# Kernel tuning notes

Hardware: AMD Instinct MI355X
Metric: run time of the kernel (lower is better)

Reference implementation:

```python
import jax, jax.numpy as jnp
import numpy as np

C = 128

def setup_inputs() -> dict:
    key = jax.random.key(0)
    ks = jax.random.split(key, 7)
    x = jax.random.normal(ks[0], (4, 64, 64, C), dtype=jnp.float32)
    s = 1.0 / np.sqrt(C)
    Wq = jax.random.normal(ks[1], (C, C), dtype=jnp.float32) * s
    bq = jnp.zeros((C,), dtype=jnp.float32)
    Wk = jax.random.normal(ks[2], (C, C), dtype=jnp.float32) * s
    bk = jnp.zeros((C,), dtype=jnp.float32)
    Wv = jax.random.normal(ks[3], (C, C), dtype=jnp.float32) * s
    bv = jnp.zeros((C,), dtype=jnp.float32)
    return {"x": x, "Wq": Wq, "bq": bq, "Wk": Wk, "bk": bk, "Wv": Wv, "bv": bv}

def reference(x, Wq, bq, Wk, bk, Wv, bv):
    B, H, W, Cc = x.shape
    N = H * W
    xt = x.reshape(B, N, Cc)  # 1x1 conv == per-token linear
    q = xt @ Wq + bq
    k = xt @ Wk + bk
    v = xt @ Wv + bv
    scale = jnp.sqrt(jnp.asarray(Cc, dtype=x.dtype))
    attn = jnp.einsum('bnc,bmc->bnm', q, k) / scale  # [B, N, N]
    attn = jax.nn.softmax(attn, axis=-1)
    out = jnp.einsum('bnm,bmc->bnc', attn, v)
    return x + out.reshape(B, H, W, Cc)
```

## Files before the change

kernel.cpp:

```cpp
#include <hip/hip_runtime.h>

constexpr int C       = 128;
constexpr int N       = 4096;
constexpr int BATCH   = 4;
constexpr int TOTROWS = BATCH * N;
constexpr float SCALE = 0.08838834764831845f;
constexpr float LOG2E = 1.44269504088896340736f;

constexpr int BK = 64;

typedef __attribute__((ext_vector_type(8))) short        bf16x8;
typedef __attribute__((ext_vector_type(4))) float        f32x4;
typedef __attribute__((ext_vector_type(2))) unsigned int u32x2;

__device__ inline unsigned short f2bf(float f) {
    unsigned int u = __float_as_uint(f);
    return (unsigned short)((u + 0x7FFFu + ((u >> 16) & 1u)) >> 16);
}
__device__ inline unsigned int cvtpk(float a, float b) {
    unsigned int r;
    asm("v_cvt_pk_bf16_f32 %0, %1, %2" : "=v"(r) : "v"(a), "v"(b));
    return r;
}
__device__ inline float bf2f(unsigned int u) {
    return __uint_as_float(u << 16);
}
__device__ inline float fexp2(float x) {
#if __has_builtin(__builtin_amdgcn_exp2f)
    return __builtin_amdgcn_exp2f(x);
#else
    float r; asm("v_exp_f32 %0, %1\n\ts_nop 0" : "=v"(r) : "v"(x)); return r;
#endif
}
__device__ inline void dma16(const void* g, void* l) {
    __builtin_amdgcn_global_load_lds(
        (const __attribute__((address_space(1))) void*)g,
        (__attribute__((address_space(3))) void*)l, 16, 0, 0);
}

__global__ __launch_bounds__(256)
void qkv_kernel(const float* __restrict__ x,
                const float* __restrict__ Wq, const float* __restrict__ bq,
                const float* __restrict__ Wk, const float* __restrict__ bk,
                const float* __restrict__ Wv, const float* __restrict__ bv,
                unsigned short* __restrict__ qo,
                unsigned short* __restrict__ ko,
                unsigned short* __restrict__ vt)
{
    constexpr int TS = 136;
    __shared__ __align__(16) unsigned short wl[128 * TS];

    const int tid  = threadIdx.x;
    const int wv   = tid >> 6;
    const int lane = tid & 63;
    const int lo   = lane & 15;
    const int quad = lane >> 4;
    const int mat  = blockIdx.y;
    const long rowbase = (long)blockIdx.x * 64 + wv * 16;

    const float* W    = (mat == 0) ? Wq : (mat == 1) ? Wk : Wv;
    const float* bias = (mat == 0) ? bq : (mat == 1) ? bk : bv;
    const float  s    = (mat == 0) ? SCALE * LOG2E : 1.0f;

    bf16x8 xf[4];
    {
        const float4* xr = reinterpret_cast<const float4*>(&x[(rowbase + lo) * C]);
        #pragma unroll
        for (int ks = 0; ks < 4; ++ks) {
            float4 a  = xr[ks * 8 + quad * 2];
            float4 b2 = xr[ks * 8 + quad * 2 + 1];
            union { bf16x8 v; unsigned int u[4]; } cv;
            cv.u[0] = cvtpk(a.x, a.y);
            cv.u[1] = cvtpk(a.z, a.w);
            cv.u[2] = cvtpk(b2.x, b2.y);
            cv.u[3] = cvtpk(b2.z, b2.w);
            xf[ks] = cv.v;
        }
    }

    #pragma unroll
    for (int g = 0; g < 16; ++g) {
        int idx = g * 256 + tid;
        int i = idx >> 5, c4 = (idx & 31) * 4;
        float4 a = *reinterpret_cast<const float4*>(&W[i * 128 + c4]);
        wl[(c4 + 0) * TS + i] = f2bf(a.x * s);
        wl[(c4 + 1) * TS + i] = f2bf(a.y * s);
        wl[(c4 + 2) * TS + i] = f2bf(a.z * s);
        wl[(c4 + 3) * TS + i] = f2bf(a.w * s);
    }
    __syncthreads();

    if (mat < 2) {
        f32x4 acc[8] = {};
        #pragma unroll
        for (int ks = 0; ks < 4; ++ks)
            #pragma unroll
            for (int mt = 0; mt < 8; ++mt) {
                bf16x8 wf = *reinterpret_cast<const bf16x8*>(
                    &wl[(mt * 16 + lo) * TS + ks * 32 + quad * 8]);
                acc[mt] = __builtin_amdgcn_mfma_f32_16x16x32_bf16(
                    wf, xf[ks], acc[mt], 0, 0, 0);
            }
        unsigned short* out = (mat == 0) ? qo : ko;
        long row = rowbase + lo;
        #pragma unroll
        for (int mt = 0; mt < 8; ++mt) {
            float4 bb = *reinterpret_cast<const float4*>(&bias[mt * 16 + quad * 4]);
            u32x2 w;
            w[0] = cvtpk(acc[mt][0] + bb.x * s, acc[mt][1] + bb.y * s);
            w[1] = cvtpk(acc[mt][2] + bb.z * s, acc[mt][3] + bb.w * s);
            *reinterpret_cast<u32x2*>(&out[row * C + mt * 16 + quad * 4]) = w;
        }
    } else {
        f32x4 acc[8] = {};
        #pragma unroll
        for (int ks = 0; ks < 4; ++ks)
            #pragma unroll
            for (int ct = 0; ct < 8; ++ct) {
                bf16x8 wf = *reinterpret_cast<const bf16x8*>(
                    &wl[(ct * 16 + lo) * TS + ks * 32 + quad * 8]);
                acc[ct] = __builtin_amdgcn_mfma_f32_16x16x32_bf16(
                    xf[ks], wf, acc[ct], 0, 0, 0);
            }
        const int b = (int)(rowbase >> 12);
        const int nbase = (int)(rowbase & (N - 1));
        const int n0   = nbase + quad * 4;
        const int nblk = n0 >> 6;
        #pragma unroll
        for (int ct = 0; ct < 8; ++ct) {
            int chan = ct * 16 + lo;
            float bb = bias[chan];
            u32x2 w;
            w[0] = cvtpk(acc[ct][0] + bb, acc[ct][1] + bb);
            w[1] = cvtpk(acc[ct][2] + bb, acc[ct][3] + bb);
            *reinterpret_cast<u32x2*>(
                &vt[(((size_t)b * 64 + nblk) * 128 + chan) * 64 + (n0 & 63)]) = w;
        }
    }
}

__global__ __launch_bounds__(256, 2)
void attn_kernel(const unsigned short* __restrict__ q,
                 const unsigned short* __restrict__ k,
                 const unsigned short* __restrict__ vt,
                 unsigned short* __restrict__ opart,
                 float* __restrict__ lpart)
{
    __shared__ __align__(16) unsigned short smA[17472];
    __shared__ __align__(16) unsigned short smB[16384];
    __shared__ __align__(16) unsigned short smP[4096];

    const int tid  = threadIdx.x;
    const int wv   = tid >> 6;
    const int lane = tid & 63;
    const int lo   = lane & 15;
    const int quad = lane >> 4;

    const int nspl = (int)(gridDim.x >> 7);
    const int id   = blockIdx.x;
    int b, sl, qt;
    if (nspl == 4) {
        b  = (id >> 1) & 3;
        sl = (id & 1) | (((id >> 3) & 1) << 1);
        qt = id >> 4;
    } else {
        b  = (id >> 1) & 3;
        sl = id & 1;
        qt = id >> 3;
    }
    const int NIT  = (N / nspl) / BK;
    const int koff = sl * (N / nspl);

    const int    rowb  = b * N + qt * 128;
    const size_t qrow0 = (size_t)rowb + wv * 32;
    const unsigned short* kb  = k  + ((size_t)b * N + koff) * C;
    const unsigned short* vtb = vt + ((size_t)b * 64 + (koff >> 6)) * (size_t)(128 * 64);
    const char* kb8 = (const char*)kb;
    const char* vb8 = (const char*)vtb;

    unsigned short* PW = smP + wv * 1024;

    bf16x8 qf[2][4];
    #pragma unroll
    for (int nt = 0; nt < 2; ++nt)
        #pragma unroll
        for (int ks = 0; ks < 4; ++ks)
            qf[nt][ks] = *reinterpret_cast<const bf16x8*>(
                &q[(qrow0 + nt * 16 + lo) * C + ks * 32 + quad * 8]);

    int offK[4], offV[4];
    #pragma unroll
    for (int c = 0; c < 4; ++c) {
        int G  = (wv * 4 + c) * 64 + lane;
        int kr = G >> 4;
        offK[c] = kr * 256 + (((G & 15) ^ (kr & 7)) << 4);
        int vr = G >> 3;
        offV[c] = vr * 128 + (((G & 7) ^ (vr & 7)) << 4);
    }

    auto stage = [&](int kt, unsigned short* dstKV) {
        const char* kt8 = kb8 + kt * 16384;
        const char* vt8 = vb8 + kt * 16384;
        #pragma unroll
        for (int c = 0; c < 4; ++c)
            dma16(kt8 + offK[c], dstKV + (wv * 4 + c) * 512);
        #pragma unroll
        for (int c = 0; c < 4; ++c)
            dma16(vt8 + offV[c], dstKV + 8192 + (wv * 4 + c) * 512);
    };

    float l_i[2] = { 0.f, 0.f };
    f32x4 ot[2][8] = {};

    auto body = [&](const unsigned short* base) {
        const unsigned short* kc = base;
        const unsigned short* vc = base + 8192;

        f32x4 st[4][2] = {};
        #pragma unroll
        for (int ks = 0; ks < 4; ++ks)
            #pragma unroll
            for (int mt = 0; mt < 4; ++mt) {
                const bf16x8 kf = *reinterpret_cast<const bf16x8*>(
                    &kc[(mt * 16 + lo) * 128 + (((ks * 4 + quad) ^ (lo & 7)) << 3)]);
                #pragma unroll
                for (int nt = 0; nt < 2; ++nt)
                    st[mt][nt] = __builtin_amdgcn_mfma_f32_16x16x32_bf16(
                        kf, qf[nt][ks], st[mt][nt], 0, 0, 0);
            }

        #pragma unroll
        for (int h = 0; h < 2; ++h) {
            #pragma unroll
            for (int nt = 0; nt < 2; ++nt) {
                const int prow = nt * 16 + lo;
                float ps = 0.f;
                #pragma unroll
                for (int m = 0; m < 2; ++m) {
                    f32x4 s = st[2 * h + m][nt];
                    float p0 = fexp2(s[0]);
                    float p1 = fexp2(s[1]);
                    float p2 = fexp2(s[2]);
                    float p3 = fexp2(s[3]);
                    ps += (p0 + p1) + (p2 + p3);
                    u32x2 w;
                    w[0] = cvtpk(p0, p1);
                    w[1] = cvtpk(p2, p3);
                    *reinterpret_cast<u32x2*>(
                        &PW[prow * 32 + (((2 * m + (quad >> 1)) ^ (prow & 3)) << 3)
                            + (quad & 1) * 4]) = w;
                }
                l_i[nt] += ps;
            }
            bf16x8 pf[2];
            #pragma unroll
            for (int nt = 0; nt < 2; ++nt) {
                const int prow = nt * 16 + lo;
                pf[nt] = *reinterpret_cast<const bf16x8*>(
                    &PW[prow * 32 + ((quad ^ (prow & 3)) << 3)]);
            }
            #pragma unroll
            for (int ct = 0; ct < 8; ++ct) {
                const bf16x8 vf = *reinterpret_cast<const bf16x8*>(
                    &vc[(ct * 16 + lo) * 64 + (((h * 4 + quad) ^ (lo & 7)) << 3)]);
                #pragma unroll
                for (int nt = 0; nt < 2; ++nt)
                    ot[nt][ct] = __builtin_amdgcn_mfma_f32_16x16x32_bf16(
                        vf, pf[nt], ot[nt][ct], 0, 0, 0);
            }
        }
    };

    stage(0, smA);
    __syncthreads();
    for (int kt = 0; kt < NIT; kt += 2) {
        stage(kt + 1, smB);
        body(smA);
        __syncthreads();
        if (kt + 2 < NIT) stage(kt + 2, smA);
        body(smB);
        __syncthreads();
    }

    #pragma unroll
    for (int nt = 0; nt < 2; ++nt) {
        l_i[nt] += __shfl_xor(l_i[nt], 16);
        l_i[nt] += __shfl_xor(l_i[nt], 32);
    }
    if (quad == 0) {
        #pragma unroll
        for (int nt = 0; nt < 2; ++nt)
            lpart[(size_t)sl * TOTROWS + qrow0 + nt * 16 + lo] = l_i[nt];
    }

    constexpr int OSTR = 136;
    unsigned short* obl = smA;
    #pragma unroll
    for (int nt = 0; nt < 2; ++nt) {
        const int row = wv * 32 + nt * 16 + lo;
        #pragma unroll
        for (int ct = 0; ct < 8; ++ct) {
            u32x2 w;
            w[0] = cvtpk(ot[nt][ct][0], ot[nt][ct][1]);
            w[1] = cvtpk(ot[nt][ct][2], ot[nt][ct][3]);
            *reinterpret_cast<u32x2*>(&obl[row * OSTR + ct * 16 + quad * 4]) = w;
        }
    }
    __syncthreads();
    {
        unsigned short* obg = opart + (size_t)sl * TOTROWS * C;
        const int row  = tid >> 1;
        const int half = tid & 1;
        const unsigned short* src = &obl[row * OSTR + half * 64];
        unsigned short*       dst = &obg[((size_t)rowb + row) * C + half * 64];
        #pragma unroll
        for (int i = 0; i < 8; ++i)
            *reinterpret_cast<uint4*>(&dst[i * 8]) =
                *reinterpret_cast<const uint4*>(&src[i * 8]);
    }
}

__global__ __launch_bounds__(256)
void combine_kernel(const float* __restrict__ x,
                    const unsigned short* __restrict__ opart,
                    const float* __restrict__ lpart,
                    float* __restrict__ out, int nspl)
{
    int gid = blockIdx.x * 256 + threadIdx.x;
    int row = gid >> 5;
    int c4  = (gid & 31) * 4;

    float denom = 0.f;
    for (int j = 0; j < nspl; ++j) denom += lpart[(size_t)j * TOTROWS + row];
    float inv = 1.0f / denom;

    size_t idx = (size_t)row * C + c4;
    float a0 = 0.f, a1 = 0.f, a2 = 0.f, a3 = 0.f;
    for (int j = 0; j < nspl; ++j) {
        u32x2 o = *reinterpret_cast<const u32x2*>(
            &opart[(size_t)j * TOTROWS * C + idx]);
        a0 += bf2f(o[0] & 0xffff);
        a1 += bf2f(o[0] >> 16);
        a2 += bf2f(o[1] & 0xffff);
        a3 += bf2f(o[1] >> 16);
    }
    float4 xv = *reinterpret_cast<const float4*>(&x[idx]);
    float4 o;
    o.x = xv.x + a0 * inv;
    o.y = xv.y + a1 * inv;
    o.z = xv.z + a2 * inv;
    o.w = xv.w + a3 * inv;
    *reinterpret_cast<float4*>(&out[idx]) = o;
}

extern "C" void kernel_launch(void* const* d_in, const int* in_sizes, int n_in,
                              void* d_out, int out_size, void* d_ws, size_t ws_size,
                              hipStream_t stream)
{
    const float* x  = (const float*)d_in[0];
    const float* Wq = (const float*)d_in[1];
    const float* bq = (const float*)d_in[2];
    const float* Wk = (const float*)d_in[3];
    const float* bk = (const float*)d_in[4];
    const float* Wv = (const float*)d_in[5];
    const float* bv = (const float*)d_in[6];
    float* out = (float*)d_out;

    const int nspl = (ws_size >= ((size_t)31 << 20)) ? 4 : 2;

    const size_t SPLIT_BYTES = (size_t)TOTROWS * C * 2;
    char* ws = (char*)d_ws;
    unsigned short* opart = (unsigned short*)ws;
    char* base = ws + (size_t)nspl * SPLIT_BYTES;
    unsigned short* q  = (unsigned short*)(base);
    unsigned short* k  = (unsigned short*)(base + SPLIT_BYTES);
    unsigned short* vt = (unsigned short*)(base + 2 * SPLIT_BYTES);
    float*          lp = (float*)(base + 3 * SPLIT_BYTES);

    qkv_kernel<<<dim3(TOTROWS / 64, 3), 256, 0, stream>>>(
        x, Wq, bq, Wk, bk, Wv, bv, q, k, vt);
    attn_kernel<<<nspl * 128, 256, 0, stream>>>(q, k, vt, opart, lp);
    combine_kernel<<<TOTROWS * 32 / 256, 256, 0, stream>>>(x, opart, lp, out, nspl);
}
```

Measured before the change: 133.1 us.

## Shrink attention K/V tile, raise occupancy, add 8-way split and swizzled weight LDS

The attention kernel's key tile drops from 64 to 32 keys, and its LDS footprint shrinks to one 40KB buffer so four blocks per CU fit (launch bounds 256,4). Setprio hints are placed around the MFMA sections, and an 8-way key split is added when the workspace is large enough. The QKV kernel switches its padded weight LDS layout to an XOR-swizzled unpadded one. The aim is more parallelism and latency hiding, at the cost of more sync overhead per key, tighter register limits and more partial outputs for the combine kernel to merge.

```diff
diff --git a/kernel.cpp b/kernel.cpp
--- a/kernel.cpp
+++ b/kernel.cpp
@@ -7,7 +7,7 @@
 constexpr float SCALE = 0.08838834764831845f;
 constexpr float LOG2E = 1.44269504088896340736f;
 
-constexpr int BK = 64;
+constexpr int BK = 32;
 
 typedef __attribute__((ext_vector_type(8))) short        bf16x8;
 typedef __attribute__((ext_vector_type(4))) float        f32x4;
@@ -47,16 +47,14 @@
                 unsigned short* __restrict__ ko,
                 unsigned short* __restrict__ vt)
 {
-    constexpr int TS = 136;
-    __shared__ __align__(16) unsigned short wl[128 * TS];
+    __shared__ __align__(16) unsigned short wl[128 * 128];
 
     const int tid  = threadIdx.x;
-    const int wv   = tid >> 6;
     const int lane = tid & 63;
     const int lo   = lane & 15;
     const int quad = lane >> 4;
     const int mat  = blockIdx.y;
-    const long rowbase = (long)blockIdx.x * 64 + wv * 16;
+    const long rowbase = (long)blockIdx.x * 64 + (tid >> 6) * 16;
 
     const float* W    = (mat == 0) ? Wq : (mat == 1) ? Wk : Wv;
     const float* bias = (mat == 0) ? bq : (mat == 1) ? bk : bv;
@@ -83,10 +81,12 @@
         int idx = g * 256 + tid;
         int i = idx >> 5, c4 = (idx & 31) * 4;
         float4 a = *reinterpret_cast<const float4*>(&W[i * 128 + c4]);
-        wl[(c4 + 0) * TS + i] = f2bf(a.x * s);
-        wl[(c4 + 1) * TS + i] = f2bf(a.y * s);
-        wl[(c4 + 2) * TS + i] = f2bf(a.z * s);
-        wl[(c4 + 3) * TS + i] = f2bf(a.w * s);
+        float v[4] = { a.x * s, a.y * s, a.z * s, a.w * s };
+        #pragma unroll
+        for (int j = 0; j < 4; ++j) {
+            int r = c4 + j;
+            wl[r * 128 + (((i >> 3) ^ ((r >> 2) & 7)) << 3) + (i & 7)] = f2bf(v[j]);
+        }
     }
     __syncthreads();
 
@@ -96,8 +96,9 @@
         for (int ks = 0; ks < 4; ++ks)
             #pragma unroll
             for (int mt = 0; mt < 8; ++mt) {
+                const int rr = mt * 16 + lo;
                 bf16x8 wf = *reinterpret_cast<const bf16x8*>(
-                    &wl[(mt * 16 + lo) * TS + ks * 32 + quad * 8]);
+                    &wl[rr * 128 + (((ks * 4 + quad) ^ ((rr >> 2) & 7)) << 3)]);
                 acc[mt] = __builtin_amdgcn_mfma_f32_16x16x32_bf16(
                     wf, xf[ks], acc[mt], 0, 0, 0);
             }
@@ -117,8 +118,9 @@
         for (int ks = 0; ks < 4; ++ks)
             #pragma unroll
             for (int ct = 0; ct < 8; ++ct) {
+                const int rr = ct * 16 + lo;
                 bf16x8 wf = *reinterpret_cast<const bf16x8*>(
-                    &wl[(ct * 16 + lo) * TS + ks * 32 + quad * 8]);
+                    &wl[rr * 128 + (((ks * 4 + quad) ^ ((rr >> 2) & 7)) << 3)]);
                 acc[ct] = __builtin_amdgcn_mfma_f32_16x16x32_bf16(
                     xf[ks], wf, acc[ct], 0, 0, 0);
             }
@@ -139,16 +141,14 @@
     }
 }
 
-__global__ __launch_bounds__(256, 2)
+__global__ __launch_bounds__(256, 4)
 void attn_kernel(const unsigned short* __restrict__ q,
                  const unsigned short* __restrict__ k,
                  const unsigned short* __restrict__ vt,
                  unsigned short* __restrict__ opart,
                  float* __restrict__ lpart)
 {
-    __shared__ __align__(16) unsigned short smA[17472];
-    __shared__ __align__(16) unsigned short smB[16384];
-    __shared__ __align__(16) unsigned short smP[4096];
+    __shared__ __align__(16) unsigned short sm[20480];
 
     const int tid  = threadIdx.x;
     const int wv   = tid >> 6;
@@ -159,7 +159,11 @@
     const int nspl = (int)(gridDim.x >> 7);
     const int id   = blockIdx.x;
     int b, sl, qt;
-    if (nspl == 4) {
+    if (nspl == 8) {
+        b  = (id >> 1) & 3;
+        sl = (id & 1) | (((id >> 3) & 3) << 1);
+        qt = id >> 5;
+    } else if (nspl == 4) {
         b  = (id >> 1) & 3;
         sl = (id & 1) | (((id >> 3) & 1) << 1);
         qt = id >> 4;
@@ -173,12 +177,10 @@
 
     const int    rowb  = b * N + qt * 128;
     const size_t qrow0 = (size_t)rowb + wv * 32;
-    const unsigned short* kb  = k  + ((size_t)b * N + koff) * C;
-    const unsigned short* vtb = vt + ((size_t)b * 64 + (koff >> 6)) * (size_t)(128 * 64);
-    const char* kb8 = (const char*)kb;
-    const char* vb8 = (const char*)vtb;
-
-    unsigned short* PW = smP + wv * 1024;
+    const char* kb8 = (const char*)(k  + ((size_t)b * N + koff) * C);
+    const char* vb8 = (const char*)(vt + ((size_t)b * 64 + (koff >> 6)) * (size_t)(128 * 64));
+
+    unsigned short* PW = sm + 16384 + wv * 1024;
 
     bf16x8 qf[2][4];
     #pragma unroll
@@ -188,25 +190,25 @@
             qf[nt][ks] = *reinterpret_cast<const bf16x8*>(
                 &q[(qrow0 + nt * 16 + lo) * C + ks * 32 + quad * 8]);
 
-    int offK[4], offV[4];
-    #pragma unroll
-    for (int c = 0; c < 4; ++c) {
-        int G  = (wv * 4 + c) * 64 + lane;
+    int offK[2], offV[2];
+    #pragma unroll
+    for (int c = 0; c < 2; ++c) {
+        int G  = c * 256 + tid;
         int kr = G >> 4;
         offK[c] = kr * 256 + (((G & 15) ^ (kr & 7)) << 4);
-        int vr = G >> 3;
-        offV[c] = vr * 128 + (((G & 7) ^ (vr & 7)) << 4);
-    }
-
-    auto stage = [&](int kt, unsigned short* dstKV) {
-        const char* kt8 = kb8 + kt * 16384;
-        const char* vt8 = vb8 + kt * 16384;
-        #pragma unroll
-        for (int c = 0; c < 4; ++c)
-            dma16(kt8 + offK[c], dstKV + (wv * 4 + c) * 512);
-        #pragma unroll
-        for (int c = 0; c < 4; ++c)
-            dma16(vt8 + offV[c], dstKV + 8192 + (wv * 4 + c) * 512);
+        int vr = G >> 2;
+        offV[c] = vr * 128 + (((G & 3) ^ (vr & 3)) << 4);
+    }
+
+    auto stage = [&](int kt, unsigned short* dst) {
+        const char* ksrc = kb8 + kt * 8192;
+        const char* vsrc = vb8 + (kt >> 1) * 16384 + (kt & 1) * 64;
+        #pragma unroll
+        for (int c = 0; c < 2; ++c)
+            dma16(ksrc + offK[c], dst + (c * 256 + tid) * 8);
+        #pragma unroll
+        for (int c = 0; c < 2; ++c)
+            dma16(vsrc + offV[c], dst + 4096 + (c * 256 + tid) * 8);
     };
 
     float l_i[2] = { 0.f, 0.f };
@@ -214,13 +216,14 @@
 
     auto body = [&](const unsigned short* base) {
         const unsigned short* kc = base;
-        const unsigned short* vc = base + 8192;
-
-        f32x4 st[4][2] = {};
+        const unsigned short* vc = base + 4096;
+
+        f32x4 st[2][2] = {};
+        __builtin_amdgcn_s_setprio(1);
         #pragma unroll
         for (int ks = 0; ks < 4; ++ks)
             #pragma unroll
-            for (int mt = 0; mt < 4; ++mt) {
+            for (int mt = 0; mt < 2; ++mt) {
                 const bf16x8 kf = *reinterpret_cast<const bf16x8*>(
                     &kc[(mt * 16 + lo) * 128 + (((ks * 4 + quad) ^ (lo & 7)) << 3)]);
                 #pragma unroll
@@ -228,57 +231,59 @@
                     st[mt][nt] = __builtin_amdgcn_mfma_f32_16x16x32_bf16(
                         kf, qf[nt][ks], st[mt][nt], 0, 0, 0);
             }
-
-        #pragma unroll
-        for (int h = 0; h < 2; ++h) {
-            #pragma unroll
-            for (int nt = 0; nt < 2; ++nt) {
-                const int prow = nt * 16 + lo;
-                float ps = 0.f;
-                #pragma unroll
-                for (int m = 0; m < 2; ++m) {
-                    f32x4 s = st[2 * h + m][nt];
-                    float p0 = fexp2(s[0]);
-                    float p1 = fexp2(s[1]);
-                    float p2 = fexp2(s[2]);
-                    float p3 = fexp2(s[3]);
-                    ps += (p0 + p1) + (p2 + p3);
-                    u32x2 w;
-                    w[0] = cvtpk(p0, p1);
-                    w[1] = cvtpk(p2, p3);
-                    *reinterpret_cast<u32x2*>(
-                        &PW[prow * 32 + (((2 * m + (quad >> 1)) ^ (prow & 3)) << 3)
-                            + (quad & 1) * 4]) = w;
-                }
-                l_i[nt] += ps;
+        __builtin_amdgcn_s_setprio(0);
+
+        #pragma unroll
+        for (int nt = 0; nt < 2; ++nt) {
+            const int prow = nt * 16 + lo;
+            float ps = 0.f;
+            #pragma unroll
+            for (int mt = 0; mt < 2; ++mt) {
+                f32x4 sv = st[mt][nt];
+                float p0 = fexp2(sv[0]);
+                float p1 = fexp2(sv[1]);
+                float p2 = fexp2(sv[2]);
+                float p3 = fexp2(sv[3]);
+                ps += (p0 + p1) + (p2 + p3);
+                u32x2 w;
+                w[0] = cvtpk(p0, p1);
+                w[1] = cvtpk(p2, p3);
+                *reinterpret_cast<u32x2*>(
+                    &PW[prow * 32 + (((mt * 2 + (quad >> 1)) ^ (prow & 3)) << 3)
+                        + (quad & 1) * 4]) = w;
             }
-            bf16x8 pf[2];
-            #pragma unroll
-            for (int nt = 0; nt < 2; ++nt) {
-                const int prow = nt * 16 + lo;
-                pf[nt] = *reinterpret_cast<const bf16x8*>(
-                    &PW[prow * 32 + ((quad ^ (prow & 3)) << 3)]);
-            }
-            #pragma unroll
-            for (int ct = 0; ct < 8; ++ct) {
-                const bf16x8 vf = *reinterpret_cast<const bf16x8*>(
-                    &vc[(ct * 16 + lo) * 64 + (((h * 4 + quad) ^ (lo & 7)) << 3)]);
-                #pragma unroll
-                for (int nt = 0; nt < 2; ++nt)
-                    ot[nt][ct] = __builtin_amdgcn_mfma_f32_16x16x32_bf16(
-                        vf, pf[nt], ot[nt][ct], 0, 0, 0);
-            }
-        }
+            l_i[nt] += ps;
+        }
+
+        bf16x8 pf[2];
+        #pragma unroll
+        for (int nt = 0; nt < 2; ++nt) {
+            const int prow = nt * 16 + lo;
+            pf[nt] = *reinterpret_cast<const bf16x8*>(
+                &PW[prow * 32 + ((quad ^ (prow & 3)) << 3)]);
+        }
+        __builtin_amdgcn_s_setprio(1);
+        #pragma unroll
+        for (int ct = 0; ct < 8; ++ct) {
+            const int rv = ct * 16 + lo;
+            const bf16x8 vf = *reinterpret_cast<const bf16x8*>(
+                &vc[rv * 32 + ((quad ^ (rv & 3)) << 3)]);
+            #pragma unroll
+            for (int nt = 0; nt < 2; ++nt)
+                ot[nt][ct] = __builtin_amdgcn_mfma_f32_16x16x32_bf16(
+                    vf, pf[nt], ot[nt][ct], 0, 0, 0);
+        }
+        __builtin_amdgcn_s_setprio(0);
     };
 
-    stage(0, smA);
+    stage(0, sm);
     __syncthreads();
     for (int kt = 0; kt < NIT; kt += 2) {
-        stage(kt + 1, smB);
-        body(smA);
+        stage(kt + 1, sm + 8192);
+        body(sm);
         __syncthreads();
-        if (kt + 2 < NIT) stage(kt + 2, smA);
-        body(smB);
+        if (kt + 2 < NIT) stage(kt + 2, sm);
+        body(sm + 8192);
         __syncthreads();
     }
 
@@ -294,7 +299,7 @@
     }
 
     constexpr int OSTR = 136;
-    unsigned short* obl = smA;
+    unsigned short* obl = sm;
     #pragma unroll
     for (int nt = 0; nt < 2; ++nt) {
         const int row = wv * 32 + nt * 16 + lo;
@@ -366,7 +371,8 @@
     const float* bv = (const float*)d_in[6];
     float* out = (float*)d_out;
 
-    const int nspl = (ws_size >= ((size_t)31 << 20)) ? 4 : 2;
+    const int nspl = (ws_size >= ((size_t)46 << 20)) ? 8
+                   : (ws_size >= ((size_t)31 << 20)) ? 4 : 2;
 
     const size_t SPLIT_BYTES = (size_t)TOTROWS * C * 2;
     char* ws = (char*)d_ws;
```

Result: slower. 160.1 us (+20.3%).
